# Kernel optimization log

Measured on AMD Instinct MI355X. Metric: run time of the kernel, lower is better.

Reference implementation:

```python
import jax, jax.numpy as jnp
import numpy as np

N_NODES = 50000
N_EDGES = 800000
IN_DIM = 64
EDGE_DIM = 2
HID = 128
NUM_LAYERS = 4
NUM_GRAPHS = 128
BN_EPS = 1e-5


def setup_inputs() -> dict:
    key = jax.random.key(0)
    ks = jax.random.split(key, 24)
    s = 0.05
    inp = {
        "x": jax.random.normal(ks[0], (N_NODES, IN_DIM), jnp.float32),
        "edge_attr": jax.random.normal(ks[1], (N_EDGES, EDGE_DIM), jnp.float32),
        "edge_index": jax.random.randint(ks[2], (2, N_EDGES), 0, N_NODES, jnp.int32),
        "batch": jnp.sort(jax.random.randint(ks[3], (N_NODES,), 0, NUM_GRAPHS, jnp.int32)),
        # parameters
        "W_in": jax.random.normal(ks[4], (IN_DIM, HID), jnp.float32) * s,
        "b_in": jnp.zeros((HID,), jnp.float32),
        "W_e": jax.random.normal(ks[5], (EDGE_DIM, HID), jnp.float32) * s,
        "b_e": jnp.zeros((HID,), jnp.float32),
        "conv_W1": jax.random.normal(ks[6], (NUM_LAYERS, HID, HID), jnp.float32) * s,
        "conv_b1": jnp.zeros((NUM_LAYERS, HID), jnp.float32),
        "conv_W2": jax.random.normal(ks[7], (NUM_LAYERS, HID, HID), jnp.float32) * s,
        "conv_b2": jnp.zeros((NUM_LAYERS, HID), jnp.float32),
        "bn_g": jnp.ones((NUM_LAYERS, HID), jnp.float32),
        "bn_b": jnp.zeros((NUM_LAYERS, HID), jnp.float32),
        "vn_W1": jax.random.normal(ks[8], (HID, HID), jnp.float32) * s,
        "vn_b1": jnp.zeros((HID,), jnp.float32),
        "vn_W2": jax.random.normal(ks[9], (HID, HID), jnp.float32) * s,
        "vn_b2": jnp.zeros((HID,), jnp.float32),
        "cls_W1": jax.random.normal(ks[10], (HID, HID), jnp.float32) * s,
        "cls_b1": jnp.zeros((HID,), jnp.float32),
        "cls_W2": jax.random.normal(ks[11], (HID, 1), jnp.float32) * s,
        "cls_b2": jnp.zeros((1,), jnp.float32),
    }
    return inp


def reference(x, edge_attr, W_in, b_in, W_e, b_e, conv_W1, conv_b1, conv_W2, conv_b2,
              bn_g, bn_b, vn_W1, vn_b1, vn_W2, vn_b2, cls_W1, cls_b1, cls_W2, cls_b2,
              edge_index, batch):
    seg = jax.ops.segment_sum
    n = x.shape[0]
    src, dst = edge_index[0], edge_index[1]

    h = x @ W_in + b_in                      # [N, H]
    e = edge_attr @ W_e + b_e                # [E, H]
    vn = jnp.zeros((NUM_GRAPHS, HID), h.dtype)

    for i in range(NUM_LAYERS):
        h = h + vn[batch]                    # virtual-node broadcast
        # GINEConv (eps=0): msg = relu(x_j + e); aggregate-sum at dst; mlp(x_i + aggr)
        m = jax.nn.relu(h[src] + e)          # [E, H]
        aggr = seg(m, dst, num_segments=n)   # [N, H]
        z = h + aggr
        z = jax.nn.relu(z @ conv_W1[i] + conv_b1[i]) @ conv_W2[i] + conv_b2[i]
        # BatchNorm1d over node dim (batch statistics, biased variance)
        mu = jnp.mean(z, axis=0)
        var = jnp.mean(jnp.square(z - mu), axis=0)
        z = (z - mu) * jax.lax.rsqrt(var + BN_EPS) * bn_g[i] + bn_b[i]
        h = jax.nn.relu(z)                   # dropout disabled (deterministic)
        if i != NUM_LAYERS - 1:
            vn_up = seg(h, batch, num_segments=NUM_GRAPHS)   # global_add_pool
            vn = vn + (jax.nn.relu(vn_up @ vn_W1 + vn_b1) @ vn_W2 + vn_b2)

    # global_mean_pool
    counts = seg(jnp.ones((n,), h.dtype), batch, num_segments=NUM_GRAPHS)
    g = seg(h, batch, num_segments=NUM_GRAPHS) / jnp.maximum(counts, 1.0)[:, None]
    logits = (jax.nn.relu(g @ cls_W1 + cls_b1) @ cls_W2 + cls_b2).reshape(-1)
    return logits
```

## Files before the change

kernel.cpp:

```cpp
#include <hip/hip_runtime.h>

#define N_NODES 50000
#define N_EDGES 800000
#define IN_DIM 64
#define HID 128
#define NUM_LAYERS 4
#define NUM_GRAPHS 128
#define BN_EPS 1e-5f

typedef __attribute__((ext_vector_type(8))) short short8;
typedef __attribute__((ext_vector_type(4))) float f32x4;

__device__ inline unsigned short f2bf(float f) {
    unsigned int u = __float_as_uint(f);
    u += 0x7FFFu + ((u >> 16) & 1u);
    return (unsigned short)(u >> 16);
}
__device__ inline float bflo(unsigned int p) { return __uint_as_float(p << 16); }
__device__ inline float bfhi(unsigned int p) { return __uint_as_float(p & 0xFFFF0000u); }
__device__ inline float bfch(const uint4& v, int c) {
    unsigned int p = (&v.x)[c >> 1];
    return (c & 1) ? bfhi(p) : bflo(p);
}


__global__ void hist_kernel(const int* __restrict__ dst, int* __restrict__ cnt,
                            int* __restrict__ rank) {
    int base = blockIdx.x * 1024 + threadIdx.x;
#pragma unroll
    for (int u = 0; u < 4; ++u) {
        int e = base + u * 256;
        if (e < N_EDGES) rank[e] = atomicAdd(&cnt[dst[e]], 1);
    }
}

__global__ void endpos_kernel(const int* __restrict__ batch, int* __restrict__ endpos) {
    int n = blockIdx.x * 256 + threadIdx.x;
    if (n >= N_NODES) return;
    int b = batch[n];
    int b1 = (n + 1 < N_NODES) ? batch[n + 1] : NUM_GRAPHS;
    for (int g = b; g < b1; ++g) endpos[g] = n + 1;
    if (n == 0)
        for (int g = 0; g < b; ++g) endpos[g] = 0;
}

__global__ void wprep_kernel(const float* __restrict__ W_in,
                             const float* __restrict__ conv_W1,
                             const float* __restrict__ conv_W2,
                             unsigned short* __restrict__ wt_in,
                             unsigned short* __restrict__ wt1,
                             unsigned short* __restrict__ wt2) {
    int i = blockIdx.x * 256 + threadIdx.x;
    if (i < 128 * IN_DIM) {
        int c = i >> 6, k = i & 63;
        wt_in[i] = f2bf(W_in[k * HID + c]);
    }
    if (i < 4 * HID * HID) {
        int o = i & (HID * HID - 1);
        int layer = i >> 14;
        int c = o >> 7, k = o & 127;
        wt1[i] = f2bf(conv_W1[layer * HID * HID + k * HID + c]);
        wt2[i] = f2bf(conv_W2[layer * HID * HID + k * HID + c]);
    }
}

#define SCAN_BLOCKS ((N_NODES + 1023) / 1024)

__global__ __launch_bounds__(1024) void scan1_kernel(const int* __restrict__ cnt,
                                                     int* __restrict__ bsum) {
    __shared__ int ls[1024];
    int t = threadIdx.x;
    int g = blockIdx.x * 1024 + t;
    int v = (g < N_NODES) ? cnt[g] : 0;
    ls[t] = v;
    __syncthreads();
    for (int off = 512; off > 0; off >>= 1) {
        if (t < off) ls[t] += ls[t + off];
        __syncthreads();
    }
    if (t == 0) bsum[blockIdx.x] = ls[0];
}

__global__ void scan2_kernel(const int* __restrict__ bsum, int* __restrict__ boff) {
    if (threadIdx.x == 0) {
        int r = 0;
        for (int i = 0; i < SCAN_BLOCKS; ++i) {
            boff[i] = r;
            r += bsum[i];
        }
    }
}

__global__ __launch_bounds__(1024) void scan3_kernel(const int* __restrict__ cnt,
                                                     const int* __restrict__ boff,
                                                     int* __restrict__ row_start) {
    __shared__ int ls[1024];
    int t = threadIdx.x;
    int g = blockIdx.x * 1024 + t;
    int v = (g < N_NODES) ? cnt[g] : 0;
    ls[t] = v;
    __syncthreads();
    for (int off = 1; off < 1024; off <<= 1) {
        int x = (t >= off) ? ls[t - off] : 0;
        __syncthreads();
        ls[t] += x;
        __syncthreads();
    }
    int excl = ls[t] - v + boff[blockIdx.x];
    if (g < N_NODES) {
        row_start[g] = excl;
        if (g == N_NODES - 1) row_start[N_NODES] = excl + v;
    }
}

__global__ void fill_kernel(const int* __restrict__ src, const int* __restrict__ dst,
                            const float* __restrict__ ea, const int* __restrict__ rank,
                            const int* __restrict__ row_start, int4* __restrict__ edges) {
    int e = blockIdx.x * 256 + threadIdx.x;
    if (e >= N_EDGES) return;
    float2 a = *(const float2*)&ea[2 * e];
    int p = row_start[dst[e]] + rank[e];
    edges[p] = make_int4(src[e], __float_as_int(a.x), __float_as_int(a.y), 0);
}

__global__ void hvadd_kernel(const unsigned short* __restrict__ hbf,
                             const unsigned short* __restrict__ vnb,
                             const int* __restrict__ batch,
                             unsigned short* __restrict__ gbf) {
    int idx = blockIdx.x * 256 + threadIdx.x;
    int n = idx >> 4;
    if (n >= N_NODES) return;
    int cg = (idx & 15) * 8;
    uint4 h = *(const uint4*)&hbf[(size_t)n * HID + cg];
    uint4 v = *(const uint4*)&vnb[(size_t)batch[n] * HID + cg];
    unsigned int o[4];
#pragma unroll
    for (int p = 0; p < 4; ++p) {
        float lo = bflo((&h.x)[p]) + bflo((&v.x)[p]);
        float hi = bfhi((&h.x)[p]) + bfhi((&v.x)[p]);
        o[p] = (unsigned int)f2bf(lo) | ((unsigned int)f2bf(hi) << 16);
    }
    *(uint4*)&gbf[(size_t)n * HID + cg] = make_uint4(o[0], o[1], o[2], o[3]);
}

__global__ __launch_bounds__(256) void aggr_kernel(const unsigned short* __restrict__ gbf,
                                                   const int4* __restrict__ edges,
                                                   const int* __restrict__ row_start,
                                                   const float* __restrict__ We,
                                                   const float* __restrict__ be,
                                                   unsigned short* __restrict__ zbf,
                                                   float* __restrict__ S1,
                                                   float* __restrict__ S2) {
    int tid = threadIdx.x;
    if (blockIdx.x == 0 && tid < HID) {
        S1[tid] = 0.f;
        S2[tid] = 0.f;
    }
    int cg = (tid & 15) * 8;
    int n = blockIdx.x * 16 + (tid >> 4);

    float w0[8], w1[8], bc[8];
    {
        float4 a0 = *(const float4*)&We[cg], a1 = *(const float4*)&We[cg + 4];
        float4 b0 = *(const float4*)&We[HID + cg], b1v = *(const float4*)&We[HID + cg + 4];
        float4 c0 = *(const float4*)&be[cg], c1 = *(const float4*)&be[cg + 4];
        w0[0]=a0.x; w0[1]=a0.y; w0[2]=a0.z; w0[3]=a0.w; w0[4]=a1.x; w0[5]=a1.y; w0[6]=a1.z; w0[7]=a1.w;
        w1[0]=b0.x; w1[1]=b0.y; w1[2]=b0.z; w1[3]=b0.w; w1[4]=b1v.x; w1[5]=b1v.y; w1[6]=b1v.z; w1[7]=b1v.w;
        bc[0]=c0.x; bc[1]=c0.y; bc[2]=c0.z; bc[3]=c0.w; bc[4]=c1.x; bc[5]=c1.y; bc[6]=c1.z; bc[7]=c1.w;
    }

    uint4 hs = *(const uint4*)&gbf[(size_t)n * HID + cg];
    int jb = row_start[n], je = row_start[n + 1];
    float acc[8];
#pragma unroll
    for (int c = 0; c < 8; ++c) acc[c] = 0.f;

    int j = jb;
    for (; j + 8 <= je; j += 8) {
        int4 q[8];
        uint4 hq[8];
#pragma unroll
        for (int u = 0; u < 8; ++u) q[u] = edges[j + u];
#pragma unroll
        for (int u = 0; u < 8; ++u) hq[u] = *(const uint4*)&gbf[(size_t)q[u].x * HID + cg];
#pragma unroll
        for (int u = 0; u < 8; ++u) {
            float ex = __int_as_float(q[u].y), ey = __int_as_float(q[u].z);
#pragma unroll
            for (int c = 0; c < 8; ++c)
                acc[c] += fmaxf(bfch(hq[u], c) + fmaf(ex, w0[c], fmaf(ey, w1[c], bc[c])), 0.f);
        }
    }
    if (j + 4 <= je) {
        int4 q[4];
        uint4 hq[4];
#pragma unroll
        for (int u = 0; u < 4; ++u) q[u] = edges[j + u];
#pragma unroll
        for (int u = 0; u < 4; ++u) hq[u] = *(const uint4*)&gbf[(size_t)q[u].x * HID + cg];
#pragma unroll
        for (int u = 0; u < 4; ++u) {
            float ex = __int_as_float(q[u].y), ey = __int_as_float(q[u].z);
#pragma unroll
            for (int c = 0; c < 8; ++c)
                acc[c] += fmaxf(bfch(hq[u], c) + fmaf(ex, w0[c], fmaf(ey, w1[c], bc[c])), 0.f);
        }
        j += 4;
    }
    for (; j < je; ++j) {
        int4 q = edges[j];
        uint4 hq = *(const uint4*)&gbf[(size_t)q.x * HID + cg];
        float ex = __int_as_float(q.y), ey = __int_as_float(q.z);
#pragma unroll
        for (int c = 0; c < 8; ++c)
            acc[c] += fmaxf(bfch(hq, c) + fmaf(ex, w0[c], fmaf(ey, w1[c], bc[c])), 0.f);
    }

    unsigned int o[4];
#pragma unroll
    for (int p = 0; p < 4; ++p)
        o[p] = (unsigned int)f2bf(bflo((&hs.x)[p]) + acc[2 * p]) |
               ((unsigned int)f2bf(bfhi((&hs.x)[p]) + acc[2 * p + 1]) << 16);
    *(uint4*)&zbf[(size_t)n * HID + cg] = make_uint4(o[0], o[1], o[2], o[3]);
}

__global__ __launch_bounds__(256) void ingemm_kernel(const float* __restrict__ A,
                                                     const unsigned short* __restrict__ Wt,
                                                     const float* __restrict__ bias,
                                                     unsigned short* __restrict__ outbf) {
    constexpr int KD = IN_DIM;
    __shared__ unsigned short aS[64 * KD];
    __shared__ unsigned short wS[128 * KD];
    int tid = threadIdx.x;
    int row0 = blockIdx.x * 64;

#pragma unroll
    for (int it = 0; it < (64 * KD) / (256 * 4); ++it) {
        int idx = it * 1024 + tid * 4;
        int r = idx / KD, k = idx % KD;
        int grow = row0 + r;
        float4 v = (grow < N_NODES) ? *(const float4*)&A[(size_t)grow * KD + k]
                                    : make_float4(0.f, 0.f, 0.f, 0.f);
        unsigned int d0 = (unsigned int)f2bf(v.x) | ((unsigned int)f2bf(v.y) << 16);
        unsigned int d1 = (unsigned int)f2bf(v.z) | ((unsigned int)f2bf(v.w) << 16);
        unsigned int byte = (unsigned int)(idx * 2) ^ (unsigned int)((r & 7) << 4);
        *(uint2*)((char*)aS + byte) = make_uint2(d0, d1);
    }
#pragma unroll
    for (int it = 0; it < (128 * KD) / (256 * 8); ++it) {
        int idx = it * 2048 + tid * 8;
        int c = idx / KD;
        uint4 v = *(const uint4*)&Wt[idx];
        unsigned int byte = (unsigned int)(idx * 2) ^ (unsigned int)((c & 7) << 4);
        *(uint4*)((char*)wS + byte) = v;
    }
    __syncthreads();

    int w = tid >> 6, l = tid & 63;
    int wr = w >> 1, wc = w & 1, lr = l & 15, kq = (l >> 4) * 8;
    f32x4 acc[2][4];
#pragma unroll
    for (int r = 0; r < 2; ++r)
#pragma unroll
        for (int t = 0; t < 4; ++t) acc[r][t] = (f32x4){0.f, 0.f, 0.f, 0.f};

#pragma unroll
    for (int sstep = 0; sstep < KD / 32; ++sstep) {
        int k0 = sstep * 32 + kq;
        int ar0 = 32 * wr + lr, ar1 = ar0 + 16;
        short8 af0 = *(short8*)((char*)aS + ((unsigned int)((ar0 * KD + k0) * 2) ^
                                            (unsigned int)((ar0 & 7) << 4)));
        short8 af1 = *(short8*)((char*)aS + ((unsigned int)((ar1 * KD + k0) * 2) ^
                                            (unsigned int)((ar1 & 7) << 4)));
#pragma unroll
        for (int t = 0; t < 4; ++t) {
            int col = 64 * wc + 16 * t + lr;
            short8 bf = *(short8*)((char*)wS + ((unsigned int)((col * KD + k0) * 2) ^
                                               (unsigned int)((col & 7) << 4)));
            acc[0][t] = __builtin_amdgcn_mfma_f32_16x16x32_bf16(af0, bf, acc[0][t], 0, 0, 0);
            acc[1][t] = __builtin_amdgcn_mfma_f32_16x16x32_bf16(af1, bf, acc[1][t], 0, 0, 0);
        }
    }
#pragma unroll
    for (int r = 0; r < 2; ++r) {
        int rbase = row0 + 32 * wr + 16 * r + (l >> 4) * 4;
#pragma unroll
        for (int t = 0; t < 4; ++t) {
            int col = 64 * wc + 16 * t + lr;
            float b = bias[col];
#pragma unroll
            for (int q = 0; q < 4; ++q) {
                int grow = rbase + q;
                if (grow < N_NODES) outbf[(size_t)grow * HID + col] = f2bf(acc[r][t][q] + b);
            }
        }
    }
}

__global__ __launch_bounds__(512) void conv_kernel(const unsigned short* __restrict__ zbf,
                                                   const unsigned short* __restrict__ Wt1,
                                                   const float* __restrict__ b1,
                                                   const unsigned short* __restrict__ Wt2,
                                                   const float* __restrict__ b2,
                                                   unsigned short* __restrict__ z2bf,
                                                   float* __restrict__ S1,
                                                   float* __restrict__ S2,
                                                   float* __restrict__ zinit, int zinit_n) {
    constexpr int KD = HID;
    __shared__ unsigned short aS[128 * KD];
    __shared__ unsigned short wS[128 * KD];
    __shared__ float sh1[HID], sh2[HID];
    int tid = threadIdx.x;
    if (zinit && blockIdx.x == 0)
        for (int i = tid; i < zinit_n; i += 512) zinit[i] = 0.f;
    if (tid < HID) { sh1[tid] = 0.f; sh2[tid] = 0.f; }

    int row0 = blockIdx.x * 128;

#pragma unroll
    for (int it = 0; it < 4; ++it) {
        int idx = it * 4096 + tid * 8;
        int r = idx >> 7;
        int grow = row0 + r;
        uint4 v = (grow < N_NODES) ? *(const uint4*)&zbf[(size_t)grow * HID + (idx & 127)]
                                   : make_uint4(0u, 0u, 0u, 0u);
        unsigned int byte = (unsigned int)(idx * 2) ^ (unsigned int)((r & 7) << 4);
        *(uint4*)((char*)aS + byte) = v;
    }
#pragma unroll
    for (int it = 0; it < 4; ++it) {
        int idx = it * 4096 + tid * 8;
        int c = idx >> 7;
        uint4 v = *(const uint4*)&Wt1[idx];
        unsigned int byte = (unsigned int)(idx * 2) ^ (unsigned int)((c & 7) << 4);
        *(uint4*)((char*)wS + byte) = v;
    }
    __syncthreads();

    int w = tid >> 6, l = tid & 63;
    int wr = w >> 2, wc = w & 3;
    int lr = l & 15, kq = (l >> 4) * 8;

    f32x4 acc[4][2];
#pragma unroll
    for (int rt = 0; rt < 4; ++rt)
#pragma unroll
        for (int ct = 0; ct < 2; ++ct) acc[rt][ct] = (f32x4){0.f, 0.f, 0.f, 0.f};

#pragma unroll
    for (int sstep = 0; sstep < 4; ++sstep) {
        int k0 = sstep * 32 + kq;
        short8 af[4];
#pragma unroll
        for (int rt = 0; rt < 4; ++rt) {
            int ar = 64 * wr + 16 * rt + lr;
            af[rt] = *(short8*)((char*)aS + ((unsigned int)((ar * KD + k0) * 2) ^
                                            (unsigned int)((ar & 7) << 4)));
        }
#pragma unroll
        for (int ct = 0; ct < 2; ++ct) {
            int col = 32 * wc + 16 * ct + lr;
            short8 bf = *(short8*)((char*)wS + ((unsigned int)((col * KD + k0) * 2) ^
                                               (unsigned int)((col & 7) << 4)));
#pragma unroll
            for (int rt = 0; rt < 4; ++rt)
                acc[rt][ct] = __builtin_amdgcn_mfma_f32_16x16x32_bf16(af[rt], bf, acc[rt][ct], 0, 0, 0);
        }
    }
    __syncthreads();

#pragma unroll
    for (int rt = 0; rt < 4; ++rt) {
        int lrow0 = 64 * wr + 16 * rt + (l >> 4) * 4;
#pragma unroll
        for (int ct = 0; ct < 2; ++ct) {
            int col = 32 * wc + 16 * ct + lr;
            float b = b1[col];
#pragma unroll
            for (int q = 0; q < 4; ++q) {
                int lrow = lrow0 + q;
                float v = fmaxf(acc[rt][ct][q] + b, 0.f);
                unsigned int byte = (unsigned int)((lrow * KD + col) * 2) ^
                                    (unsigned int)((lrow & 7) << 4);
                *(unsigned short*)((char*)aS + byte) = f2bf(v);
            }
        }
    }
#pragma unroll
    for (int it = 0; it < 4; ++it) {
        int idx = it * 4096 + tid * 8;
        int c = idx >> 7;
        uint4 v = *(const uint4*)&Wt2[idx];
        unsigned int byte = (unsigned int)(idx * 2) ^ (unsigned int)((c & 7) << 4);
        *(uint4*)((char*)wS + byte) = v;
    }
    __syncthreads();

    f32x4 acc2[4][2];
#pragma unroll
    for (int rt = 0; rt < 4; ++rt)
#pragma unroll
        for (int ct = 0; ct < 2; ++ct) acc2[rt][ct] = (f32x4){0.f, 0.f, 0.f, 0.f};

#pragma unroll
    for (int sstep = 0; sstep < 4; ++sstep) {
        int k0 = sstep * 32 + kq;
        short8 af[4];
#pragma unroll
        for (int rt = 0; rt < 4; ++rt) {
            int ar = 64 * wr + 16 * rt + lr;
            af[rt] = *(short8*)((char*)aS + ((unsigned int)((ar * KD + k0) * 2) ^
                                            (unsigned int)((ar & 7) << 4)));
        }
#pragma unroll
        for (int ct = 0; ct < 2; ++ct) {
            int col = 32 * wc + 16 * ct + lr;
            short8 bf = *(short8*)((char*)wS + ((unsigned int)((col * KD + k0) * 2) ^
                                               (unsigned int)((col & 7) << 4)));
#pragma unroll
            for (int rt = 0; rt < 4; ++rt)
                acc2[rt][ct] = __builtin_amdgcn_mfma_f32_16x16x32_bf16(af[rt], bf, acc2[rt][ct], 0, 0, 0);
        }
    }

    float s1v[2] = {0.f, 0.f}, s2v[2] = {0.f, 0.f};
#pragma unroll
    for (int rt = 0; rt < 4; ++rt) {
        int rbase = row0 + 64 * wr + 16 * rt + (l >> 4) * 4;
#pragma unroll
        for (int ct = 0; ct < 2; ++ct) {
            int col = 32 * wc + 16 * ct + lr;
            float b = b2[col];
#pragma unroll
            for (int q = 0; q < 4; ++q) {
                int grow = rbase + q;
                if (grow < N_NODES) {
                    float v = acc2[rt][ct][q] + b;
                    z2bf[(size_t)grow * HID + col] = f2bf(v);
                    s1v[ct] += v;
                    s2v[ct] += v * v;
                }
            }
        }
    }
#pragma unroll
    for (int ct = 0; ct < 2; ++ct) {
        float a = s1v[ct], bsum2 = s2v[ct];
        a += __shfl_xor(a, 16); a += __shfl_xor(a, 32);
        bsum2 += __shfl_xor(bsum2, 16); bsum2 += __shfl_xor(bsum2, 32);
        if ((l >> 4) == 0) {
            int col = 32 * wc + 16 * ct + lr;
            atomicAdd(&sh1[col], a);
            atomicAdd(&sh2[col], bsum2);
        }
    }
    __syncthreads();
    if (tid < HID) {
        atomicAdd(&S1[tid], sh1[tid]);
        atomicAdd(&S2[tid], sh2[tid]);
    }
}

__global__ __launch_bounds__(256) void bn_kernel(const unsigned short* __restrict__ z2bf,
                                                 const float* __restrict__ S1,
                                                 const float* __restrict__ S2,
                                                 const float* __restrict__ gma,
                                                 const float* __restrict__ bta,
                                                 const int* __restrict__ batch,
                                                 unsigned short* __restrict__ hbf,
                                                 float* __restrict__ up) {
    int tid = threadIdx.x;
    int cg = (tid & 31) * 4;
    int n0 = (blockIdx.x * 8 + (tid >> 5)) * 16;
    const float inv = 1.f / (float)N_NODES;
    float4 s1 = *(const float4*)&S1[cg];
    float4 s2 = *(const float4*)&S2[cg];
    float4 g4 = *(const float4*)&gma[cg];
    float4 b4 = *(const float4*)&bta[cg];
    float mux = s1.x * inv, muy = s1.y * inv, muz = s1.z * inv, muw = s1.w * inv;
    float gmx = g4.x * rsqrtf(s2.x * inv - mux * mux + BN_EPS);
    float gmy = g4.y * rsqrtf(s2.y * inv - muy * muy + BN_EPS);
    float gmz = g4.z * rsqrtf(s2.z * inv - muz * muz + BN_EPS);
    float gmw = g4.w * rsqrtf(s2.w * inv - muw * muw + BN_EPS);

    float4 acc = make_float4(0.f, 0.f, 0.f, 0.f);
    int gcur = -1;
    for (int i = 0; i < 16; ++i) {
        int n = n0 + i;
        if (n >= N_NODES) break;
        uint2 zv = *(const uint2*)&z2bf[(size_t)n * HID + cg];
        float4 hn;
        hn.x = fmaxf(fmaf(bflo(zv.x) - mux, gmx, b4.x), 0.f);
        hn.y = fmaxf(fmaf(bfhi(zv.x) - muy, gmy, b4.y), 0.f);
        hn.z = fmaxf(fmaf(bflo(zv.y) - muz, gmz, b4.z), 0.f);
        hn.w = fmaxf(fmaf(bfhi(zv.y) - muw, gmw, b4.w), 0.f);
        uint2 pk;
        pk.x = (unsigned int)f2bf(hn.x) | ((unsigned int)f2bf(hn.y) << 16);
        pk.y = (unsigned int)f2bf(hn.z) | ((unsigned int)f2bf(hn.w) << 16);
        *(uint2*)&hbf[(size_t)n * HID + cg] = pk;
        int gb = batch[n];
        if (gb != gcur) {
            if (gcur >= 0) {
                atomicAdd(&up[gcur * HID + cg + 0], acc.x);
                atomicAdd(&up[gcur * HID + cg + 1], acc.y);
                atomicAdd(&up[gcur * HID + cg + 2], acc.z);
                atomicAdd(&up[gcur * HID + cg + 3], acc.w);
            }
            acc = make_float4(0.f, 0.f, 0.f, 0.f);
            gcur = gb;
        }
        acc.x += hn.x; acc.y += hn.y; acc.z += hn.z; acc.w += hn.w;
    }
    if (gcur >= 0) {
        atomicAdd(&up[gcur * HID + cg + 0], acc.x);
        atomicAdd(&up[gcur * HID + cg + 1], acc.y);
        atomicAdd(&up[gcur * HID + cg + 2], acc.z);
        atomicAdd(&up[gcur * HID + cg + 3], acc.w);
    }
}

__global__ __launch_bounds__(128) void vnmlp_kernel(const float* __restrict__ up,
                                                    const float* __restrict__ W1,
                                                    const float* __restrict__ b1,
                                                    const float* __restrict__ W2,
                                                    const float* __restrict__ b2,
                                                    float* __restrict__ vn,
                                                    unsigned short* __restrict__ vnb) {
    __shared__ float t[HID];
    int g = blockIdx.x, c = threadIdx.x;
    float s = b1[c];
#pragma unroll 8
    for (int k = 0; k < HID; ++k) s = fmaf(up[g * HID + k], W1[k * HID + c], s);
    t[c] = fmaxf(s, 0.f);
    __syncthreads();
    float s2 = b2[c];
#pragma unroll 8
    for (int k = 0; k < HID; ++k) s2 = fmaf(t[k], W2[k * HID + c], s2);
    float nv = vn[g * HID + c] + s2;
    vn[g * HID + c] = nv;
    vnb[g * HID + c] = f2bf(nv);
}

__global__ __launch_bounds__(128) void cls_kernel(const float* __restrict__ pool,
                                                  const int* __restrict__ endpos,
                                                  const float* __restrict__ W1,
                                                  const float* __restrict__ b1,
                                                  const float* __restrict__ W2,
                                                  const float* __restrict__ b2,
                                                  float* __restrict__ out) {
    __shared__ float t[HID];
    __shared__ float red[HID];
    int g = blockIdx.x, c = threadIdx.x;
    int cnt = endpos[g] - (g > 0 ? endpos[g - 1] : 0);
    float cntf = fmaxf((float)cnt, 1.f);
    t[c] = pool[g * HID + c] / cntf;
    __syncthreads();
    float s = b1[c];
#pragma unroll 8
    for (int k = 0; k < HID; ++k) s = fmaf(t[k], W1[k * HID + c], s);
    float y = fmaxf(s, 0.f);
    red[c] = y * W2[c];
    __syncthreads();
    for (int off = 64; off > 0; off >>= 1) {
        if (c < off) red[c] += red[c + off];
        __syncthreads();
    }
    if (c == 0) out[g] = red[0] + b2[0];
}

extern "C" void kernel_launch(void* const* d_in, const int* in_sizes, int n_in,
                              void* d_out, int out_size, void* d_ws, size_t ws_size,
                              hipStream_t stream) {
    const float* x        = (const float*)d_in[0];
    const float* edge_attr= (const float*)d_in[1];
    const int*   edge_idx = (const int*)d_in[2];
    const int*   batch    = (const int*)d_in[3];
    const float* W_in     = (const float*)d_in[4];
    const float* b_in     = (const float*)d_in[5];
    const float* W_e      = (const float*)d_in[6];
    const float* b_e      = (const float*)d_in[7];
    const float* conv_W1  = (const float*)d_in[8];
    const float* conv_b1  = (const float*)d_in[9];
    const float* conv_W2  = (const float*)d_in[10];
    const float* conv_b2  = (const float*)d_in[11];
    const float* bn_g     = (const float*)d_in[12];
    const float* bn_b     = (const float*)d_in[13];
    const float* vn_W1    = (const float*)d_in[14];
    const float* vn_b1    = (const float*)d_in[15];
    const float* vn_W2    = (const float*)d_in[16];
    const float* vn_b2    = (const float*)d_in[17];
    const float* cls_W1   = (const float*)d_in[18];
    const float* cls_b1   = (const float*)d_in[19];
    const float* cls_W2   = (const float*)d_in[20];
    const float* cls_b2   = (const float*)d_in[21];

    char* ws = (char*)d_ws;
    size_t off = 0;
    auto alloc = [&](size_t bytes) -> void* {
        void* p = ws + off;
        off = (off + bytes + 255) & ~(size_t)255;
        return p;
    };
    unsigned short* z2bf = (unsigned short*)alloc((size_t)N_NODES * HID * 2);
    unsigned short* hbf = (unsigned short*)alloc((size_t)N_NODES * HID * 2);
    unsigned short* gbf = (unsigned short*)alloc((size_t)N_NODES * HID * 2);
    unsigned short* zbf = (unsigned short*)alloc((size_t)N_NODES * HID * 2);
    size_t zero_begin = off;
    int*   cnt    = (int*)alloc((size_t)N_NODES * 4);
    float* vn     = (float*)alloc((size_t)NUM_GRAPHS * HID * 4);
    unsigned short* vnb = (unsigned short*)alloc((size_t)NUM_GRAPHS * HID * 2);
    float* pool   = (float*)alloc((size_t)NUM_GRAPHS * HID * 4);
    size_t zero_end = off;
    int*    endpos    = (int*)alloc((size_t)NUM_GRAPHS * 4);
    int*    row_start = (int*)alloc((size_t)(N_NODES + 1) * 4);
    int*    rank      = (int*)alloc((size_t)N_EDGES * 4);
    int4*   edges     = (int4*)alloc((size_t)N_EDGES * 16);
    float*  vn_up     = (float*)alloc((size_t)NUM_GRAPHS * HID * 4);
    float*  S1        = (float*)alloc((size_t)HID * 4);
    float*  S2        = (float*)alloc((size_t)HID * 4);
    int*    bsum      = (int*)alloc((size_t)SCAN_BLOCKS * 4);
    int*    boff      = (int*)alloc((size_t)SCAN_BLOCKS * 4);
    unsigned short* wt_in = (unsigned short*)alloc((size_t)HID * IN_DIM * 2);
    unsigned short* wt1   = (unsigned short*)alloc((size_t)NUM_LAYERS * HID * HID * 2);
    unsigned short* wt2   = (unsigned short*)alloc((size_t)NUM_LAYERS * HID * HID * 2);
    (void)ws_size; (void)in_sizes; (void)n_in; (void)out_size;

    const int* srcp = edge_idx;
    const int* dstp = edge_idx + N_EDGES;

    hipMemsetAsync(ws + zero_begin, 0, zero_end - zero_begin, stream);
    hist_kernel<<<(N_EDGES + 1023) / 1024, 256, 0, stream>>>(dstp, cnt, rank);
    endpos_kernel<<<(N_NODES + 255) / 256, 256, 0, stream>>>(batch, endpos);
    wprep_kernel<<<(4 * HID * HID + 255) / 256, 256, 0, stream>>>(W_in, conv_W1, conv_W2,
                                                                  wt_in, wt1, wt2);
    scan1_kernel<<<SCAN_BLOCKS, 1024, 0, stream>>>(cnt, bsum);
    scan2_kernel<<<1, 64, 0, stream>>>(bsum, boff);
    scan3_kernel<<<SCAN_BLOCKS, 1024, 0, stream>>>(cnt, boff, row_start);
    fill_kernel<<<(N_EDGES + 255) / 256, 256, 0, stream>>>(srcp, dstp, edge_attr, rank,
                                                           row_start, edges);

    ingemm_kernel<<<(N_NODES + 63) / 64, 256, 0, stream>>>(x, wt_in, b_in, hbf);

    const int conv_grid = (N_NODES + 127) / 128;
    for (int i = 0; i < NUM_LAYERS; ++i) {
        const unsigned short* src_tab = hbf;
        if (i > 0) {
            hvadd_kernel<<<(N_NODES * 16 + 255) / 256, 256, 0, stream>>>(hbf, vnb, batch, gbf);
            src_tab = gbf;
        }
        aggr_kernel<<<N_NODES / 16, 256, 0, stream>>>(src_tab, edges, row_start,
                                                      W_e, b_e, zbf, S1, S2);
        conv_kernel<<<conv_grid, 512, 0, stream>>>(
            zbf, wt1 + (size_t)i * HID * HID, conv_b1 + (size_t)i * HID,
            wt2 + (size_t)i * HID * HID, conv_b2 + (size_t)i * HID,
            z2bf, S1, S2, (i < NUM_LAYERS - 1) ? vn_up : nullptr, NUM_GRAPHS * HID);
        bn_kernel<<<(N_NODES + 127) / 128, 256, 0, stream>>>(z2bf, S1, S2, bn_g + (size_t)i * HID,
                                                             bn_b + (size_t)i * HID, batch, hbf,
                                                             (i < NUM_LAYERS - 1) ? vn_up : pool);
        if (i < NUM_LAYERS - 1)
            vnmlp_kernel<<<NUM_GRAPHS, 128, 0, stream>>>(vn_up, vn_W1, vn_b1, vn_W2, vn_b2,
                                                         vn, vnb);
    }

    cls_kernel<<<NUM_GRAPHS, 128, 0, stream>>>(pool, endpos, cls_W1, cls_b1, cls_W2, cls_b2,
                                               (float*)d_out);
}
```

Measured before the change: 431.5 us.

## Split each node's edge aggregation across four lane groups with shuffle reduction

The aggregation kernel now assigns a full 64-lane wavefront per destination node instead of 16 lanes. The four 16-lane subgroups each take a different edge within every group of four and combine their partial sums with xor shuffles before one subgroup writes the result. This gives more parallelism and memory-level parallelism for the gather, and shortens the serial per-node loop for skewed degrees. In exchange it launches four times as many blocks, keeps fewer loads in flight per thread, and adds shuffle reduction cost.

```diff
diff --git a/kernel.cpp b/kernel.cpp
--- a/kernel.cpp
+++ b/kernel.cpp
@@ -156,8 +156,10 @@
         S1[tid] = 0.f;
         S2[tid] = 0.f;
     }
-    int cg = (tid & 15) * 8;
-    int n = blockIdx.x * 16 + (tid >> 4);
+    int l = tid & 63;
+    int n = blockIdx.x * 4 + (tid >> 6);
+    int cg = (l & 15) * 8;
+    int u = l >> 4;
 
     float w0[8], w1[8], bc[8];
     {
@@ -177,51 +179,50 @@
 
     int j = jb;
     for (; j + 8 <= je; j += 8) {
-        int4 q[8];
-        uint4 hq[8];
-#pragma unroll
-        for (int u = 0; u < 8; ++u) q[u] = edges[j + u];
-#pragma unroll
-        for (int u = 0; u < 8; ++u) hq[u] = *(const uint4*)&gbf[(size_t)q[u].x * HID + cg];
-#pragma unroll
-        for (int u = 0; u < 8; ++u) {
-            float ex = __int_as_float(q[u].y), ey = __int_as_float(q[u].z);
-#pragma unroll
-            for (int c = 0; c < 8; ++c)
-                acc[c] += fmaxf(bfch(hq[u], c) + fmaf(ex, w0[c], fmaf(ey, w1[c], bc[c])), 0.f);
+        int4 q0 = edges[j + u];
+        int4 q1 = edges[j + 4 + u];
+        uint4 h0 = *(const uint4*)&gbf[(size_t)q0.x * HID + cg];
+        uint4 h1 = *(const uint4*)&gbf[(size_t)q1.x * HID + cg];
+        float e0x = __int_as_float(q0.y), e0y = __int_as_float(q0.z);
+        float e1x = __int_as_float(q1.y), e1y = __int_as_float(q1.z);
+#pragma unroll
+        for (int c = 0; c < 8; ++c) {
+            acc[c] += fmaxf(bfch(h0, c) + fmaf(e0x, w0[c], fmaf(e0y, w1[c], bc[c])), 0.f);
+            acc[c] += fmaxf(bfch(h1, c) + fmaf(e1x, w0[c], fmaf(e1y, w1[c], bc[c])), 0.f);
         }
     }
     if (j + 4 <= je) {
-        int4 q[4];
-        uint4 hq[4];
-#pragma unroll
-        for (int u = 0; u < 4; ++u) q[u] = edges[j + u];
-#pragma unroll
-        for (int u = 0; u < 4; ++u) hq[u] = *(const uint4*)&gbf[(size_t)q[u].x * HID + cg];
-#pragma unroll
-        for (int u = 0; u < 4; ++u) {
-            float ex = __int_as_float(q[u].y), ey = __int_as_float(q[u].z);
-#pragma unroll
-            for (int c = 0; c < 8; ++c)
-                acc[c] += fmaxf(bfch(hq[u], c) + fmaf(ex, w0[c], fmaf(ey, w1[c], bc[c])), 0.f);
-        }
-        j += 4;
-    }
-    for (; j < je; ++j) {
-        int4 q = edges[j];
+        int4 q = edges[j + u];
         uint4 hq = *(const uint4*)&gbf[(size_t)q.x * HID + cg];
         float ex = __int_as_float(q.y), ey = __int_as_float(q.z);
 #pragma unroll
         for (int c = 0; c < 8; ++c)
             acc[c] += fmaxf(bfch(hq, c) + fmaf(ex, w0[c], fmaf(ey, w1[c], bc[c])), 0.f);
-    }
-
-    unsigned int o[4];
-#pragma unroll
-    for (int p = 0; p < 4; ++p)
-        o[p] = (unsigned int)f2bf(bflo((&hs.x)[p]) + acc[2 * p]) |
-               ((unsigned int)f2bf(bfhi((&hs.x)[p]) + acc[2 * p + 1]) << 16);
-    *(uint4*)&zbf[(size_t)n * HID + cg] = make_uint4(o[0], o[1], o[2], o[3]);
+        j += 4;
+    }
+    if (u < je - j) {
+        int4 q = edges[j + u];
+        uint4 hq = *(const uint4*)&gbf[(size_t)q.x * HID + cg];
+        float ex = __int_as_float(q.y), ey = __int_as_float(q.z);
+#pragma unroll
+        for (int c = 0; c < 8; ++c)
+            acc[c] += fmaxf(bfch(hq, c) + fmaf(ex, w0[c], fmaf(ey, w1[c], bc[c])), 0.f);
+    }
+
+#pragma unroll
+    for (int c = 0; c < 8; ++c) {
+        acc[c] += __shfl_xor(acc[c], 16);
+        acc[c] += __shfl_xor(acc[c], 32);
+    }
+
+    if (u == 0) {
+        unsigned int o[4];
+#pragma unroll
+        for (int p = 0; p < 4; ++p)
+            o[p] = (unsigned int)f2bf(bflo((&hs.x)[p]) + acc[2 * p]) |
+                   ((unsigned int)f2bf(bfhi((&hs.x)[p]) + acc[2 * p + 1]) << 16);
+        *(uint4*)&zbf[(size_t)n * HID + cg] = make_uint4(o[0], o[1], o[2], o[3]);
+    }
 }
 
 __global__ __launch_bounds__(256) void ingemm_kernel(const float* __restrict__ A,
@@ -648,8 +649,8 @@
             hvadd_kernel<<<(N_NODES * 16 + 255) / 256, 256, 0, stream>>>(hbf, vnb, batch, gbf);
             src_tab = gbf;
         }
-        aggr_kernel<<<N_NODES / 16, 256, 0, stream>>>(src_tab, edges, row_start,
-                                                      W_e, b_e, zbf, S1, S2);
+        aggr_kernel<<<N_NODES / 4, 256, 0, stream>>>(src_tab, edges, row_start,
+                                                     W_e, b_e, zbf, S1, S2);
         conv_kernel<<<conv_grid, 512, 0, stream>>>(
             zbf, wt1 + (size_t)i * HID * HID, conv_b1 + (size_t)i * HID,
             wt2 + (size_t)i * HID * HID, conv_b2 + (size_t)i * HID,
```

Measured after the change: 446.7 us. 1.04x slower.

## Merge prep kernels, fold scan2 into scan3, pack edges to 8 bytes

Applied to the files above, without the earlier changes.

Merges the histogram, endpos and weight-prep kernels into one launch. Scan2 is removed, and each scan3 block now computes its own block offset with a wavefront shuffle reduction. Edge records shrink from 16 to 8 bytes by storing the two edge attributes as bf16, which halves edge-list traffic in the per-layer aggregation. The cost is lower precision on the edge attributes and fewer kernel launches to hide latency.

```diff
diff --git a/kernel.cpp b/kernel.cpp
--- a/kernel.cpp
+++ b/kernel.cpp
@@ -23,34 +23,29 @@
     return (c & 1) ? bfhi(p) : bflo(p);
 }
 
-
-__global__ void hist_kernel(const int* __restrict__ dst, int* __restrict__ cnt,
-                            int* __restrict__ rank) {
-    int base = blockIdx.x * 1024 + threadIdx.x;
+__global__ void prep_kernel(const int* __restrict__ dst, int* __restrict__ cnt,
+                            int* __restrict__ rank, const int* __restrict__ batch,
+                            int* __restrict__ endpos, const float* __restrict__ W_in,
+                            const float* __restrict__ conv_W1,
+                            const float* __restrict__ conv_W2,
+                            unsigned short* __restrict__ wt_in,
+                            unsigned short* __restrict__ wt1,
+                            unsigned short* __restrict__ wt2) {
+    int tid = threadIdx.x;
+    int base = blockIdx.x * 1024 + tid;
 #pragma unroll
     for (int u = 0; u < 4; ++u) {
         int e = base + u * 256;
         if (e < N_EDGES) rank[e] = atomicAdd(&cnt[dst[e]], 1);
     }
-}
-
-__global__ void endpos_kernel(const int* __restrict__ batch, int* __restrict__ endpos) {
-    int n = blockIdx.x * 256 + threadIdx.x;
-    if (n >= N_NODES) return;
-    int b = batch[n];
-    int b1 = (n + 1 < N_NODES) ? batch[n + 1] : NUM_GRAPHS;
-    for (int g = b; g < b1; ++g) endpos[g] = n + 1;
-    if (n == 0)
-        for (int g = 0; g < b; ++g) endpos[g] = 0;
-}
-
-__global__ void wprep_kernel(const float* __restrict__ W_in,
-                             const float* __restrict__ conv_W1,
-                             const float* __restrict__ conv_W2,
-                             unsigned short* __restrict__ wt_in,
-                             unsigned short* __restrict__ wt1,
-                             unsigned short* __restrict__ wt2) {
-    int i = blockIdx.x * 256 + threadIdx.x;
+    int i = blockIdx.x * 256 + tid;
+    if (i < N_NODES) {
+        int b = batch[i];
+        int b1 = (i + 1 < N_NODES) ? batch[i + 1] : NUM_GRAPHS;
+        for (int g = b; g < b1; ++g) endpos[g] = i + 1;
+        if (i == 0)
+            for (int g = 0; g < b; ++g) endpos[g] = 0;
+    }
     if (i < 128 * IN_DIM) {
         int c = i >> 6, k = i & 63;
         wt_in[i] = f2bf(W_in[k * HID + c]);
@@ -81,21 +76,18 @@
     if (t == 0) bsum[blockIdx.x] = ls[0];
 }
 
-__global__ void scan2_kernel(const int* __restrict__ bsum, int* __restrict__ boff) {
-    if (threadIdx.x == 0) {
-        int r = 0;
-        for (int i = 0; i < SCAN_BLOCKS; ++i) {
-            boff[i] = r;
-            r += bsum[i];
-        }
-    }
-}
-
 __global__ __launch_bounds__(1024) void scan3_kernel(const int* __restrict__ cnt,
-                                                     const int* __restrict__ boff,
+                                                     const int* __restrict__ bsum,
                                                      int* __restrict__ row_start) {
     __shared__ int ls[1024];
+    __shared__ int boffS;
     int t = threadIdx.x;
+    if (t < 64) {
+        int v2 = (t < blockIdx.x && t < SCAN_BLOCKS) ? bsum[t] : 0;
+#pragma unroll
+        for (int off = 32; off > 0; off >>= 1) v2 += __shfl_down(v2, off);
+        if (t == 0) boffS = v2;
+    }
     int g = blockIdx.x * 1024 + t;
     int v = (g < N_NODES) ? cnt[g] : 0;
     ls[t] = v;
@@ -106,7 +98,7 @@
         ls[t] += x;
         __syncthreads();
     }
-    int excl = ls[t] - v + boff[blockIdx.x];
+    int excl = ls[t] - v + boffS;
     if (g < N_NODES) {
         row_start[g] = excl;
         if (g == N_NODES - 1) row_start[N_NODES] = excl + v;
@@ -115,12 +107,13 @@
 
 __global__ void fill_kernel(const int* __restrict__ src, const int* __restrict__ dst,
                             const float* __restrict__ ea, const int* __restrict__ rank,
-                            const int* __restrict__ row_start, int4* __restrict__ edges) {
+                            const int* __restrict__ row_start, int2* __restrict__ edges) {
     int e = blockIdx.x * 256 + threadIdx.x;
     if (e >= N_EDGES) return;
     float2 a = *(const float2*)&ea[2 * e];
     int p = row_start[dst[e]] + rank[e];
-    edges[p] = make_int4(src[e], __float_as_int(a.x), __float_as_int(a.y), 0);
+    unsigned int pk = (unsigned int)f2bf(a.x) | ((unsigned int)f2bf(a.y) << 16);
+    edges[p] = make_int2(src[e], (int)pk);
 }
 
 __global__ void hvadd_kernel(const unsigned short* __restrict__ hbf,
@@ -144,7 +137,7 @@
 }
 
 __global__ __launch_bounds__(256) void aggr_kernel(const unsigned short* __restrict__ gbf,
-                                                   const int4* __restrict__ edges,
+                                                   const int2* __restrict__ edges,
                                                    const int* __restrict__ row_start,
                                                    const float* __restrict__ We,
                                                    const float* __restrict__ be,
@@ -177,7 +170,7 @@
 
     int j = jb;
     for (; j + 8 <= je; j += 8) {
-        int4 q[8];
+        int2 q[8];
         uint4 hq[8];
 #pragma unroll
         for (int u = 0; u < 8; ++u) q[u] = edges[j + u];
@@ -185,14 +178,14 @@
         for (int u = 0; u < 8; ++u) hq[u] = *(const uint4*)&gbf[(size_t)q[u].x * HID + cg];
 #pragma unroll
         for (int u = 0; u < 8; ++u) {
-            float ex = __int_as_float(q[u].y), ey = __int_as_float(q[u].z);
+            float ex = bflo((unsigned int)q[u].y), ey = bfhi((unsigned int)q[u].y);
 #pragma unroll
             for (int c = 0; c < 8; ++c)
                 acc[c] += fmaxf(bfch(hq[u], c) + fmaf(ex, w0[c], fmaf(ey, w1[c], bc[c])), 0.f);
         }
     }
     if (j + 4 <= je) {
-        int4 q[4];
+        int2 q[4];
         uint4 hq[4];
 #pragma unroll
         for (int u = 0; u < 4; ++u) q[u] = edges[j + u];
@@ -200,7 +193,7 @@
         for (int u = 0; u < 4; ++u) hq[u] = *(const uint4*)&gbf[(size_t)q[u].x * HID + cg];
 #pragma unroll
         for (int u = 0; u < 4; ++u) {
-            float ex = __int_as_float(q[u].y), ey = __int_as_float(q[u].z);
+            float ex = bflo((unsigned int)q[u].y), ey = bfhi((unsigned int)q[u].y);
 #pragma unroll
             for (int c = 0; c < 8; ++c)
                 acc[c] += fmaxf(bfch(hq[u], c) + fmaf(ex, w0[c], fmaf(ey, w1[c], bc[c])), 0.f);
@@ -208,9 +201,9 @@
         j += 4;
     }
     for (; j < je; ++j) {
-        int4 q = edges[j];
+        int2 q = edges[j];
         uint4 hq = *(const uint4*)&gbf[(size_t)q.x * HID + cg];
-        float ex = __int_as_float(q.y), ey = __int_as_float(q.z);
+        float ex = bflo((unsigned int)q.y), ey = bfhi((unsigned int)q.y);
 #pragma unroll
         for (int c = 0; c < 8; ++c)
             acc[c] += fmaxf(bfch(hq, c) + fmaf(ex, w0[c], fmaf(ey, w1[c], bc[c])), 0.f);
@@ -614,12 +607,11 @@
     int*    endpos    = (int*)alloc((size_t)NUM_GRAPHS * 4);
     int*    row_start = (int*)alloc((size_t)(N_NODES + 1) * 4);
     int*    rank      = (int*)alloc((size_t)N_EDGES * 4);
-    int4*   edges     = (int4*)alloc((size_t)N_EDGES * 16);
+    int2*   edges     = (int2*)alloc((size_t)N_EDGES * 8);
     float*  vn_up     = (float*)alloc((size_t)NUM_GRAPHS * HID * 4);
     float*  S1        = (float*)alloc((size_t)HID * 4);
     float*  S2        = (float*)alloc((size_t)HID * 4);
     int*    bsum      = (int*)alloc((size_t)SCAN_BLOCKS * 4);
-    int*    boff      = (int*)alloc((size_t)SCAN_BLOCKS * 4);
     unsigned short* wt_in = (unsigned short*)alloc((size_t)HID * IN_DIM * 2);
     unsigned short* wt1   = (unsigned short*)alloc((size_t)NUM_LAYERS * HID * HID * 2);
     unsigned short* wt2   = (unsigned short*)alloc((size_t)NUM_LAYERS * HID * HID * 2);
@@ -629,13 +621,11 @@
     const int* dstp = edge_idx + N_EDGES;
 
     hipMemsetAsync(ws + zero_begin, 0, zero_end - zero_begin, stream);
-    hist_kernel<<<(N_EDGES + 1023) / 1024, 256, 0, stream>>>(dstp, cnt, rank);
-    endpos_kernel<<<(N_NODES + 255) / 256, 256, 0, stream>>>(batch, endpos);
-    wprep_kernel<<<(4 * HID * HID + 255) / 256, 256, 0, stream>>>(W_in, conv_W1, conv_W2,
-                                                                  wt_in, wt1, wt2);
+    prep_kernel<<<(N_EDGES + 1023) / 1024, 256, 0, stream>>>(dstp, cnt, rank, batch, endpos,
+                                                             W_in, conv_W1, conv_W2,
+                                                             wt_in, wt1, wt2);
     scan1_kernel<<<SCAN_BLOCKS, 1024, 0, stream>>>(cnt, bsum);
-    scan2_kernel<<<1, 64, 0, stream>>>(bsum, boff);
-    scan3_kernel<<<SCAN_BLOCKS, 1024, 0, stream>>>(cnt, boff, row_start);
+    scan3_kernel<<<SCAN_BLOCKS, 1024, 0, stream>>>(cnt, bsum, row_start);
     fill_kernel<<<(N_EDGES + 255) / 256, 256, 0, stream>>>(srcp, dstp, edge_attr, rank,
                                                            row_start, edges);
 
```

Measured after the change: 506.7 us. 1.17x slower.
